# Performance work log

Hardware: AMD Instinct MI355X
Metric: run time of the kernel (lower is better)

Reference implementation:

```python
import jax, jax.numpy as jnp
import numpy as np
import math

N_NODES = 50000
N_EDGES = 800000
F_IN = 32
HID = 64


def _layernorm(x, g, b, eps=1e-5):
    mu = x.mean(-1, keepdims=True)
    var = ((x - mu) ** 2).mean(-1, keepdims=True)
    return (x - mu) / jnp.sqrt(var + eps) * g + b


def _tconv(x, src, dst, Wq, bq, Wk, bk, Wv, bv, Ws, heads):
    # PyG TransformerConv (concat=True, root_weight=True, bias=False on skip)
    N = x.shape[0]
    C = Wq.shape[1] // heads
    q = (x @ Wq + bq).reshape(N, heads, C)[dst]  # [E,H,C] gathered at targets
    k = (x @ Wk + bk).reshape(N, heads, C)[src]  # [E,H,C] gathered at sources
    v = (x @ Wv + bv).reshape(N, heads, C)[src]
    scores = (q * k).sum(-1) / math.sqrt(C)      # [E,H]
    m = jax.ops.segment_max(scores, dst, num_segments=N)   # [N,H]
    p = jnp.exp(scores - m[dst])
    denom = jax.ops.segment_sum(p, dst, num_segments=N)
    alpha = p / (denom[dst] + 1e-16)             # segment softmax over in-edges
    agg = jax.ops.segment_sum(v * alpha[..., None], dst, num_segments=N)
    return agg.reshape(N, heads * C) + x @ Ws    # + skip (no bias)


def setup_inputs() -> dict:
    key = jax.random.key(0)
    ks = iter(jax.random.split(key, 64))
    def rn(shape, s=0.1):
        return jax.random.normal(next(ks), shape, jnp.float32) * s
    inp = {
        "x": rn((N_NODES, F_IN), 1.0),
        "edge_index": jax.random.randint(next(ks), (2, N_EDGES), 0, N_NODES, dtype=jnp.int32),
        "ln0_g": jnp.ones((F_IN,), jnp.float32),
        "ln0_b": jnp.zeros((F_IN,), jnp.float32),
    }
    dims = [F_IN, HID, HID]
    for l in range(3):
        d = dims[l]
        inp[f"Wq{l}"] = rn((d, HID)); inp[f"bq{l}"] = rn((HID,), 0.05)
        inp[f"Wk{l}"] = rn((d, HID)); inp[f"bk{l}"] = rn((HID,), 0.05)
        inp[f"Wv{l}"] = rn((d, HID)); inp[f"bv{l}"] = rn((HID,), 0.05)
        inp[f"Ws{l}"] = rn((d, HID))
        inp[f"g{l}"] = jnp.ones((HID,), jnp.float32)
        inp[f"b{l}"] = jnp.zeros((HID,), jnp.float32)
    inp["Wr1"] = rn((HID, HID // 2)); inp["br1"] = jnp.zeros((HID // 2,), jnp.float32)
    inp["Wr2"] = rn((HID // 2, 1));   inp["br2"] = jnp.zeros((1,), jnp.float32)
    inp["Wt1"] = rn((HID, HID // 2)); inp["bt1"] = jnp.zeros((HID // 2,), jnp.float32)
    inp["Wt2"] = rn((HID // 2, 1));   inp["bt2"] = jnp.zeros((1,), jnp.float32)
    return inp


def reference(x, edge_index, ln0_g, ln0_b,
              Wq0, bq0, Wk0, bk0, Wv0, bv0, Ws0, g0, b0,
              Wq1, bq1, Wk1, bk1, Wv1, bv1, Ws1, g1, b1,
              Wq2, bq2, Wk2, bk2, Wv2, bv2, Ws2, g2, b2,
              Wr1, br1, Wr2, br2, Wt1, bt1, Wt2, bt2):
    src, dst = edge_index[0], edge_index[1]
    h = _layernorm(x, ln0_g, ln0_b)
    layers = [
        (Wq0, bq0, Wk0, bk0, Wv0, bv0, Ws0, g0, b0, 4),
        (Wq1, bq1, Wk1, bk1, Wv1, bv1, Ws1, g1, b1, 4),
        (Wq2, bq2, Wk2, bk2, Wv2, bv2, Ws2, g2, b2, 1),
    ]
    for i, (Wq, bq, Wk, bk, Wv, bv, Ws, g, b, heads) in enumerate(layers):
        x_res = h if h.shape[-1] == HID else None
        h = _tconv(h, src, dst, Wq, bq, Wk, bk, Wv, bv, Ws, heads)
        h = _layernorm(h, g, b)
        if x_res is not None and i > 0:
            h = h + 0.1 * x_res
        if i < len(layers) - 1:
            h = jax.nn.relu(h)  # dropout is identity in eval mode
    rtt = jax.nn.relu(h @ Wr1 + br1) @ Wr2 + br2      # [N,1]
    retrans = jax.nn.relu(h @ Wt1 + bt1) @ Wt2 + bt2  # [N,1]
    return jnp.concatenate([rtt, retrans], axis=1)    # [N,2]
```

## Files before the change

kernel.cpp:

```cpp
#include <hip/hip_runtime.h>
#include <hip/hip_bf16.h>
#include <math.h>

#define N_NODES 50000
#define N_EDGES 800000
#define HID 64
#define NBK 196
#define EPB 1024
#define SB  782
#define FLAT (NBK * SB)
#define SCAN_B ((FLAT + 255) / 256)

#define LN0_BLKS   6250
#define HIST_BLKS  SB
#define WP0_BLKS   32
#define WP12_BLKS  64
#define PREP_BLKS  (LN0_BLKS + HIST_BLKS + WP0_BLKS + 2 * WP12_BLKS)

typedef __attribute__((ext_vector_type(8))) short short8;
typedef __attribute__((ext_vector_type(4))) float float4v;

__device__ __forceinline__ unsigned short f32_to_bf16_rne(float f) {
    unsigned int u = __float_as_uint(f);
    unsigned int r = u + 0x7fffu + ((u >> 16) & 1u);
    return (unsigned short)(r >> 16);
}

__device__ __forceinline__ void ln0_body(int b, int t,
        const float* __restrict__ x, const float* __restrict__ g,
        const float* __restrict__ bb, float* __restrict__ h0) {
    int lane = t & 63;
    int n = b * 8 + (t >> 6) * 2 + (lane >> 5);
    int c = lane & 31;
    float v = x[n * 32 + c];
    float s = v;
    #pragma unroll
    for (int off = 1; off < 32; off <<= 1) s += __shfl_xor(s, off);
    float mu = s * (1.0f / 32.0f);
    float d = v - mu;
    float vs = d * d;
    #pragma unroll
    for (int off = 1; off < 32; off <<= 1) vs += __shfl_xor(vs, off);
    float var = vs * (1.0f / 32.0f);
    h0[n * 32 + c] = d * rsqrtf(var + 1e-5f) * g[c] + bb[c];
}

__device__ __forceinline__ void wprep_body(int idx, int KS,
        const float* __restrict__ Wq, const float* __restrict__ Wk,
        const float* __restrict__ Wv, const float* __restrict__ Ws,
        unsigned short* __restrict__ Wp) {
    int j = idx & 7;
    int lane = (idx >> 3) & 63;
    int ts = idx >> 9;
    int s = ts % KS;
    int tile = ts / KS;
    int which = tile >> 2;
    int slice = tile & 3;
    int k = s * 32 + ((lane >> 4) * 8) + j;
    int col = slice * 16 + (lane & 15);
    const float* W = (which == 0) ? Wq : (which == 1) ? Wk : (which == 2) ? Wv : Ws;
    Wp[idx] = f32_to_bf16_rne(W[k * 64 + col]);
}

__global__ __launch_bounds__(256) void prep_kernel(
        const float* __restrict__ x, const float* __restrict__ ln0g,
        const float* __restrict__ ln0b, float* __restrict__ h0,
        const int* __restrict__ dst, int* __restrict__ ghist,
        const float* __restrict__ Wq0, const float* __restrict__ Wk0,
        const float* __restrict__ Wv0, const float* __restrict__ Ws0,
        unsigned short* __restrict__ Wp0,
        const float* __restrict__ Wq1, const float* __restrict__ Wk1,
        const float* __restrict__ Wv1, const float* __restrict__ Ws1,
        unsigned short* __restrict__ Wp1,
        const float* __restrict__ Wq2, const float* __restrict__ Wk2,
        const float* __restrict__ Wv2, const float* __restrict__ Ws2,
        unsigned short* __restrict__ Wp2) {
    __shared__ int hist[NBK];
    int b = blockIdx.x;
    int t = threadIdx.x;
    if (b < LN0_BLKS) {
        ln0_body(b, t, x, ln0g, ln0b, h0);
    } else if (b < LN0_BLKS + HIST_BLKS) {
        int i = b - LN0_BLKS;
        for (int k = t; k < NBK; k += 256) hist[k] = 0;
        __syncthreads();
        int e0 = i * EPB;
        #pragma unroll
        for (int r = 0; r < 4; r++) {
            int e = e0 + r * 256 + t;
            if (e < N_EDGES) atomicAdd(&hist[dst[e] >> 8], 1);
        }
        __syncthreads();
        for (int k = t; k < NBK; k += 256) ghist[k * SB + i] = hist[k];
    } else if (b < LN0_BLKS + HIST_BLKS + WP0_BLKS) {
        int idx = (b - LN0_BLKS - HIST_BLKS) * 256 + t;
        wprep_body(idx, 1, Wq0, Wk0, Wv0, Ws0, Wp0);
    } else if (b < LN0_BLKS + HIST_BLKS + WP0_BLKS + WP12_BLKS) {
        int idx = (b - LN0_BLKS - HIST_BLKS - WP0_BLKS) * 256 + t;
        wprep_body(idx, 2, Wq1, Wk1, Wv1, Ws1, Wp1);
    } else {
        int idx = (b - LN0_BLKS - HIST_BLKS - WP0_BLKS - WP12_BLKS) * 256 + t;
        wprep_body(idx, 2, Wq2, Wk2, Wv2, Ws2, Wp2);
    }
}

__global__ void scan1_kernel(const int* __restrict__ ghist, int* __restrict__ csum) {
    int f = blockIdx.x * 256 + threadIdx.x;
    int v = (f < FLAT) ? ghist[f] : 0;
    #pragma unroll
    for (int off = 1; off < 64; off <<= 1) v += __shfl_xor(v, off);
    __shared__ int ws[4];
    if ((threadIdx.x & 63) == 0) ws[threadIdx.x >> 6] = v;
    __syncthreads();
    if (threadIdx.x == 0) csum[blockIdx.x] = ws[0] + ws[1] + ws[2] + ws[3];
}

__global__ void scan2_kernel(const int* __restrict__ csum, int* __restrict__ coff,
                             int* __restrict__ bbase, int* __restrict__ row_ptr) {
    int lane = threadIdx.x;
    int carry = 0;
    for (int base = 0; base < SCAN_B; base += 64) {
        int i = base + lane;
        int v = (i < SCAN_B) ? csum[i] : 0;
        int incl = v;
        #pragma unroll
        for (int off = 1; off < 64; off <<= 1) {
            int tt = __shfl_up(incl, off);
            if (lane >= off) incl += tt;
        }
        if (i < SCAN_B) coff[i] = carry + incl - v;
        carry += __shfl(incl, 63);
    }
    if (lane == 0) { bbase[NBK] = N_EDGES; row_ptr[N_NODES] = N_EDGES; }
}

__global__ void scan3_kernel(const int* __restrict__ ghist, const int* __restrict__ coff,
                             int* __restrict__ goff, int* __restrict__ bbase) {
    int f = blockIdx.x * 256 + threadIdx.x;
    int lane = threadIdx.x & 63;
    int w = threadIdx.x >> 6;
    int v = (f < FLAT) ? ghist[f] : 0;
    int incl = v;
    #pragma unroll
    for (int off = 1; off < 64; off <<= 1) {
        int tt = __shfl_up(incl, off);
        if (lane >= off) incl += tt;
    }
    __shared__ int ws[4];
    if (lane == 63) ws[w] = incl;
    __syncthreads();
    int woff = 0;
    #pragma unroll
    for (int k = 0; k < 4; k++) if (k < w) woff += ws[k];
    int excl = coff[blockIdx.x] + woff + incl - v;
    if (f < FLAT) {
        goff[f] = excl;
        if (f % SB == 0) bbase[f / SB] = excl;
    }
}

__global__ __launch_bounds__(256) void scatter_kernel(
        const int* __restrict__ src, const int* __restrict__ dst,
        const int* __restrict__ goff, int2* __restrict__ ebkt) {
    __shared__ int hist[NBK];
    int t = threadIdx.x, i = blockIdx.x;
    for (int k = t; k < NBK; k += 256) hist[k] = 0;
    __syncthreads();
    int e0 = i * EPB;
    #pragma unroll
    for (int r = 0; r < 4; r++) {
        int e = e0 + r * 256 + t;
        if (e < N_EDGES) {
            int s = src[e], d = dst[e];
            int k = d >> 8;
            int rank = atomicAdd(&hist[k], 1);
            ebkt[goff[k * SB + i] + rank] = make_int2(s, d);
        }
    }
}

__global__ __launch_bounds__(256) void bucket_build_kernel(
        const int2* __restrict__ ebkt, const int* __restrict__ bbase,
        int* __restrict__ row_ptr, int* __restrict__ colb) {
    __shared__ int ldeg[256];
    __shared__ int lcur[256];
    __shared__ int wsum[4];
    int b = blockIdx.x;
    int t = threadIdx.x;
    int cbase = bbase[b];
    int cnt = bbase[b + 1] - cbase;
    int ebase = cbase;

    ldeg[t] = 0;
    __syncthreads();
    for (int i = t; i < cnt; i += 256) {
        int2 e = ebkt[ebase + i];
        atomicAdd(&ldeg[e.y & 255], 1);
    }
    __syncthreads();

    int lane = t & 63;
    int w = t >> 6;
    int v = ldeg[t];
    int incl = v;
    #pragma unroll
    for (int off = 1; off < 64; off <<= 1) {
        int tt = __shfl_up(incl, off);
        if (lane >= off) incl += tt;
    }
    if (lane == 63) wsum[w] = incl;
    __syncthreads();
    int woff = 0;
    #pragma unroll
    for (int k = 0; k < 4; k++) if (k < w) woff += wsum[k];
    int excl = woff + incl - v;

    int node = b * 256 + t;
    if (node < N_NODES) row_ptr[node] = cbase + excl;
    lcur[t] = excl;
    __syncthreads();

    for (int i = t; i < cnt; i += 256) {
        int2 e = ebkt[ebase + i];
        int r = atomicAdd(&lcur[e.y & 255], 1);
        colb[cbase + r] = e.x;
    }
}

template <int D>
__global__ __launch_bounds__(256) void qkvs_mfma_kernel(
        const float* __restrict__ h,
        const unsigned short* __restrict__ Wp,
        const float* __restrict__ bq, const float* __restrict__ bk,
        const float* __restrict__ bv,
        float* __restrict__ Q, unsigned int* __restrict__ KV,
        float* __restrict__ S) {
    constexpr int KS = D / 32;
    int t = threadIdx.x;
    int lane = t & 63;
    int w = t >> 6;
    int n0 = blockIdx.x * 16;
    int n16 = lane & 15;
    int quad = lane >> 4;
    int col = w * 16 + n16;

    short8 afrag[KS];
    #pragma unroll
    for (int s = 0; s < KS; s++) {
        const float* hp = &h[(n0 + n16) * D + s * 32 + quad * 8];
        float4 a0 = *(const float4*)hp;
        float4 a1 = *(const float4*)(hp + 4);
        short8 af;
        af[0] = (short)f32_to_bf16_rne(a0.x);
        af[1] = (short)f32_to_bf16_rne(a0.y);
        af[2] = (short)f32_to_bf16_rne(a0.z);
        af[3] = (short)f32_to_bf16_rne(a0.w);
        af[4] = (short)f32_to_bf16_rne(a1.x);
        af[5] = (short)f32_to_bf16_rne(a1.y);
        af[6] = (short)f32_to_bf16_rne(a1.z);
        af[7] = (short)f32_to_bf16_rne(a1.w);
        afrag[s] = af;
    }

    float4v accs[4];
    #pragma unroll
    for (int which = 0; which < 4; which++) {
        float4v acc = {0.0f, 0.0f, 0.0f, 0.0f};
        int tile = which * 4 + w;
        #pragma unroll
        for (int s = 0; s < KS; s++) {
            short8 bfrag = *(const short8*)&Wp[((tile * KS + s) * 64 + lane) * 8];
            acc = __builtin_amdgcn_mfma_f32_16x16x32_bf16(afrag[s], bfrag, acc, 0, 0, 0);
        }
        accs[which] = acc;
    }

    float bqc = bq[col], bkc = bk[col], bvc = bv[col];

    #pragma unroll
    for (int r = 0; r < 4; r++) {
        int node = n0 + quad * 4 + r;
        Q[node * 64 + col] = accs[0][r] + bqc;
        unsigned int kw = f32_to_bf16_rne(accs[1][r] + bkc);
        unsigned int vw = f32_to_bf16_rne(accs[2][r] + bvc);
        KV[node * 64 + col] = (vw << 16) | kw;
        S[node * 64 + col] = accs[3][r];
    }
}

template <int HEADS, bool RES, bool RELU, bool HEAD>
__global__ __launch_bounds__(256) void agg_kernel(
                           const float* __restrict__ Q, const unsigned int* __restrict__ KV,
                           const float* __restrict__ S,
                           const int* __restrict__ row_ptr, const int* __restrict__ colb,
                           const float* __restrict__ g, const float* __restrict__ b,
                           const float* __restrict__ h_in, float* __restrict__ h_out,
                           const float* __restrict__ Wr1, const float* __restrict__ br1,
                           const float* __restrict__ Wr2, const float* __restrict__ br2,
                           const float* __restrict__ Wt1, const float* __restrict__ bt1,
                           const float* __restrict__ Wt2, const float* __restrict__ bt2,
                           float* __restrict__ out) {
    constexpr int C = HID / HEADS;
    int lane = threadIdx.x & 63;
    int m = lane & 15;
    int grp = lane >> 4;
    int n = blockIdx.x * 4 + (threadIdx.x >> 6);

    const float scale = rsqrtf((float)C);
    float4 q4 = *(const float4*)&Q[n * 64 + 4 * m];
    q4.x *= scale; q4.y *= scale; q4.z *= scale; q4.w *= scale;

    int beg = row_ptr[n], end = row_ptr[n + 1];

    float ssum = 0.0f;
    float acc0 = 0.0f, acc1 = 0.0f, acc2 = 0.0f, acc3 = 0.0f;

    for (int base = beg; base < end; base += 64) {
        int limit = min(end - base, 64);
        int src_l = (base + lane < end) ? colb[base + lane] : 0;
        for (int sub = 0; sub < limit; sub += 16) {
            int e0 = sub + grp, e1 = sub + 4 + grp, e2 = sub + 8 + grp, e3 = sub + 12 + grp;
            int s0 = __shfl(src_l, e0);
            int s1 = __shfl(src_l, e1);
            int s2 = __shfl(src_l, e2);
            int s3 = __shfl(src_l, e3);
            bool v0ok = e0 < limit, v1ok = e1 < limit, v2ok = e2 < limit, v3ok = e3 < limit;
            uint4 kv0 = make_uint4(0, 0, 0, 0), kv1 = kv0, kv2 = kv0, kv3 = kv0;
            if (v0ok) kv0 = *(const uint4*)&KV[(size_t)s0 * 64 + 4 * m];
            if (v1ok) kv1 = *(const uint4*)&KV[(size_t)s1 * 64 + 4 * m];
            if (v2ok) kv2 = *(const uint4*)&KV[(size_t)s2 * 64 + 4 * m];
            if (v3ok) kv3 = *(const uint4*)&KV[(size_t)s3 * 64 + 4 * m];

            float t0 = fmaf(q4.x, __uint_as_float(kv0.x << 16),
                       fmaf(q4.y, __uint_as_float(kv0.y << 16),
                       fmaf(q4.z, __uint_as_float(kv0.z << 16),
                            q4.w * __uint_as_float(kv0.w << 16))));
            float t1 = fmaf(q4.x, __uint_as_float(kv1.x << 16),
                       fmaf(q4.y, __uint_as_float(kv1.y << 16),
                       fmaf(q4.z, __uint_as_float(kv1.z << 16),
                            q4.w * __uint_as_float(kv1.w << 16))));
            float t2 = fmaf(q4.x, __uint_as_float(kv2.x << 16),
                       fmaf(q4.y, __uint_as_float(kv2.y << 16),
                       fmaf(q4.z, __uint_as_float(kv2.z << 16),
                            q4.w * __uint_as_float(kv2.w << 16))));
            float t3 = fmaf(q4.x, __uint_as_float(kv3.x << 16),
                       fmaf(q4.y, __uint_as_float(kv3.y << 16),
                       fmaf(q4.z, __uint_as_float(kv3.z << 16),
                            q4.w * __uint_as_float(kv3.w << 16))));
            #pragma unroll
            for (int off = 1; off < C / 4; off <<= 1) {
                t0 += __shfl_xor(t0, off);
                t1 += __shfl_xor(t1, off);
                t2 += __shfl_xor(t2, off);
                t3 += __shfl_xor(t3, off);
            }
            float p0 = v0ok ? __expf(t0) : 0.0f;
            float p1 = v1ok ? __expf(t1) : 0.0f;
            float p2 = v2ok ? __expf(t2) : 0.0f;
            float p3 = v3ok ? __expf(t3) : 0.0f;
            ssum += (p0 + p1) + (p2 + p3);
            acc0 = fmaf(p0, __uint_as_float(kv0.x & 0xffff0000u),
                   fmaf(p1, __uint_as_float(kv1.x & 0xffff0000u),
                   fmaf(p2, __uint_as_float(kv2.x & 0xffff0000u),
                   fmaf(p3, __uint_as_float(kv3.x & 0xffff0000u), acc0))));
            acc1 = fmaf(p0, __uint_as_float(kv0.y & 0xffff0000u),
                   fmaf(p1, __uint_as_float(kv1.y & 0xffff0000u),
                   fmaf(p2, __uint_as_float(kv2.y & 0xffff0000u),
                   fmaf(p3, __uint_as_float(kv3.y & 0xffff0000u), acc1))));
            acc2 = fmaf(p0, __uint_as_float(kv0.z & 0xffff0000u),
                   fmaf(p1, __uint_as_float(kv1.z & 0xffff0000u),
                   fmaf(p2, __uint_as_float(kv2.z & 0xffff0000u),
                   fmaf(p3, __uint_as_float(kv3.z & 0xffff0000u), acc2))));
            acc3 = fmaf(p0, __uint_as_float(kv0.w & 0xffff0000u),
                   fmaf(p1, __uint_as_float(kv1.w & 0xffff0000u),
                   fmaf(p2, __uint_as_float(kv2.w & 0xffff0000u),
                   fmaf(p3, __uint_as_float(kv3.w & 0xffff0000u), acc3))));
        }
    }

    #pragma unroll
    for (int off = 16; off < 64; off <<= 1) {
        ssum += __shfl_xor(ssum, off);
        acc0 += __shfl_xor(acc0, off);
        acc1 += __shfl_xor(acc1, off);
        acc2 += __shfl_xor(acc2, off);
        acc3 += __shfl_xor(acc3, off);
    }

    float inv = 1.0f / (ssum + 1e-16f);
    float4 sv = *(const float4*)&S[n * 64 + 4 * m];
    float o0 = fmaf(acc0, inv, sv.x);
    float o1 = fmaf(acc1, inv, sv.y);
    float o2 = fmaf(acc2, inv, sv.z);
    float o3 = fmaf(acc3, inv, sv.w);

    float s = (o0 + o1) + (o2 + o3);
    #pragma unroll
    for (int off = 1; off < 16; off <<= 1) s += __shfl_xor(s, off);
    float mu = s * (1.0f / 64.0f);
    float d0 = o0 - mu, d1 = o1 - mu, d2 = o2 - mu, d3 = o3 - mu;
    float vs = (d0 * d0 + d1 * d1) + (d2 * d2 + d3 * d3);
    #pragma unroll
    for (int off = 1; off < 16; off <<= 1) vs += __shfl_xor(vs, off);
    float rstd = rsqrtf(vs * (1.0f / 64.0f) + 1e-5f);

    float4 gv = *(const float4*)&g[4 * m];
    float4 bv = *(const float4*)&b[4 * m];
    float y0 = d0 * rstd * gv.x + bv.x;
    float y1 = d1 * rstd * gv.y + bv.y;
    float y2 = d2 * rstd * gv.z + bv.z;
    float y3 = d3 * rstd * gv.w + bv.w;
    if (RES) {
        float4 rv = *(const float4*)&h_in[n * 64 + 4 * m];
        y0 = fmaf(0.1f, rv.x, y0);
        y1 = fmaf(0.1f, rv.y, y1);
        y2 = fmaf(0.1f, rv.z, y2);
        y3 = fmaf(0.1f, rv.w, y3);
    }
    if (RELU) {
        y0 = fmaxf(y0, 0.0f); y1 = fmaxf(y1, 0.0f);
        y2 = fmaxf(y2, 0.0f); y3 = fmaxf(y3, 0.0f);
    }

    if (!HEAD) {
        if (grp == 0) {
            float4 yv = make_float4(y0, y1, y2, y3);
            *(float4*)&h_out[n * 64 + 4 * m] = yv;
        }
    } else {
        __shared__ float sh[4][HID];
        int wave = threadIdx.x >> 6;
        if (grp == 0) {
            float4 yv = make_float4(y0, y1, y2, y3);
            *(float4*)&sh[wave][4 * m] = yv;
        }
        __syncthreads();
        int half = lane >> 5;
        int j = lane & 31;
        const float* W1 = half ? Wt1 : Wr1;
        const float* b1 = half ? bt1 : br1;
        const float* W2 = half ? Wt2 : Wr2;
        const float* b2v = half ? bt2 : br2;
        float a = b1[j];
        #pragma unroll 8
        for (int i = 0; i < 64; i++) a = fmaf(sh[wave][i], W1[i * 32 + j], a);
        a = fmaxf(a, 0.0f);
        float r = a * W2[j];
        #pragma unroll
        for (int off = 1; off < 32; off <<= 1) r += __shfl_xor(r, off);
        if (j == 0) out[n * 2 + half] = r + b2v[0];
    }
}

extern "C" void kernel_launch(void* const* d_in, const int* in_sizes, int n_in,
                              void* d_out, int out_size, void* d_ws, size_t ws_size,
                              hipStream_t stream) {
    const float* x    = (const float*)d_in[0];
    const int*   ei   = (const int*)d_in[1];
    const int*   src  = ei;
    const int*   dst  = ei + N_EDGES;
    const float* ln0g = (const float*)d_in[2];
    const float* ln0b = (const float*)d_in[3];

    const float* P[27];
    for (int i = 0; i < 27; i++) P[i] = (const float*)d_in[4 + i];
    const float* Wr1 = (const float*)d_in[31];
    const float* br1 = (const float*)d_in[32];
    const float* Wr2 = (const float*)d_in[33];
    const float* br2 = (const float*)d_in[34];
    const float* Wt1 = (const float*)d_in[35];
    const float* bt1 = (const float*)d_in[36];
    const float* Wt2 = (const float*)d_in[37];
    const float* bt2 = (const float*)d_in[38];

    float* out = (float*)d_out;

    float* hbuf0 = (float*)d_ws;
    float* hbuf1 = hbuf0 + N_NODES * 64;
    float* Qb    = hbuf1 + N_NODES * 64;
    float* Sb    = Qb + N_NODES * 64;
    unsigned int* KVb = (unsigned int*)(Sb + N_NODES * 64);
    int* row_ptr = (int*)(KVb + N_NODES * 64);
    int* colb    = row_ptr + (N_NODES + 1);
    int* ghist   = colb + N_EDGES;
    int* goff    = ghist + FLAT;
    int* csum    = goff + FLAT;
    int* coff    = csum + SCAN_B;
    int* bbase   = coff + SCAN_B;
    unsigned short* Wp0 = (unsigned short*)(bbase + NBK + 1);
    unsigned short* Wp1 = Wp0 + 16 * 1 * 512;
    unsigned short* Wp2 = Wp1 + 16 * 2 * 512;
    int2* ebkt = (int2*)Qb;

    prep_kernel<<<PREP_BLKS, 256, 0, stream>>>(x, ln0g, ln0b, hbuf0,
        dst, ghist,
        P[0],  P[2],  P[4],  P[6],  Wp0,
        P[9],  P[11], P[13], P[15], Wp1,
        P[18], P[20], P[22], P[24], Wp2);
    scan1_kernel<<<SCAN_B, 256, 0, stream>>>(ghist, csum);
    scan2_kernel<<<1, 64, 0, stream>>>(csum, coff, bbase, row_ptr);
    scan3_kernel<<<SCAN_B, 256, 0, stream>>>(ghist, coff, goff, bbase);
    scatter_kernel<<<SB, 256, 0, stream>>>(src, dst, goff, ebkt);
    bucket_build_kernel<<<NBK, 256, 0, stream>>>(ebkt, bbase, row_ptr, colb);

    qkvs_mfma_kernel<32><<<3125, 256, 0, stream>>>(hbuf0, Wp0,
        P[1], P[3], P[5], Qb, KVb, Sb);
    agg_kernel<4, false, true, false><<<12500, 256, 0, stream>>>(Qb, KVb, Sb,
        row_ptr, colb, P[7], P[8], nullptr, hbuf1,
        Wr1, br1, Wr2, br2, Wt1, bt1, Wt2, bt2, out);

    qkvs_mfma_kernel<64><<<3125, 256, 0, stream>>>(hbuf1, Wp1,
        P[10], P[12], P[14], Qb, KVb, Sb);
    agg_kernel<4, true, true, false><<<12500, 256, 0, stream>>>(Qb, KVb, Sb,
        row_ptr, colb, P[16], P[17], hbuf1, hbuf0,
        Wr1, br1, Wr2, br2, Wt1, bt1, Wt2, bt2, out);

    qkvs_mfma_kernel<64><<<3125, 256, 0, stream>>>(hbuf0, Wp2,
        P[19], P[21], P[23], Qb, KVb, Sb);
    agg_kernel<1, true, false, true><<<12500, 256, 0, stream>>>(Qb, KVb, Sb,
        row_ptr, colb, P[25], P[26], hbuf0, hbuf1,
        Wr1, br1, Wr2, br2, Wt1, bt1, Wt2, bt2, out);
}
```

Baseline: 338.3 us.

## Fuse next-layer QKVS MFMA projection into aggregation kernel and merge scan kernels

The aggregation kernel for layers 0 and 1 now handles 16 nodes per 1024-thread block. It stages the normalized outputs in shared memory and then runs the next layer's bf16 MFMA Q/K/V/S projection in the same kernel, writing into a second ping-pong buffer set. This removes two qkvs launches and the round trip of re-reading h from global memory. The three-kernel histogram scan is replaced by a single-block scan, and the edges-per-block count rises to 4096, which shrinks the histogram. The costs are larger blocks with a syncthreads barrier that can lower occupancy during the gather phase, extra workspace, and a serial one-block scan.

New measurement: 355.6 us. 1.05x slower.

```diff
diff --git a/kernel.cpp b/kernel.cpp
--- a/kernel.cpp
+++ b/kernel.cpp
@@ -6,10 +6,9 @@
 #define N_EDGES 800000
 #define HID 64
 #define NBK 196
-#define EPB 1024
-#define SB  782
+#define EPB 4096
+#define SB  ((N_EDGES + EPB - 1) / EPB)
 #define FLAT (NBK * SB)
-#define SCAN_B ((FLAT + 255) / 256)
 
 #define LN0_BLKS   6250
 #define HIST_BLKS  SB
@@ -86,7 +85,7 @@
         __syncthreads();
         int e0 = i * EPB;
         #pragma unroll
-        for (int r = 0; r < 4; r++) {
+        for (int r = 0; r < EPB / 256; r++) {
             int e = e0 + r * 256 + t;
             if (e < N_EDGES) atomicAdd(&hist[dst[e] >> 8], 1);
         }
@@ -104,59 +103,41 @@
     }
 }
 
-__global__ void scan1_kernel(const int* __restrict__ ghist, int* __restrict__ csum) {
-    int f = blockIdx.x * 256 + threadIdx.x;
-    int v = (f < FLAT) ? ghist[f] : 0;
-    #pragma unroll
-    for (int off = 1; off < 64; off <<= 1) v += __shfl_xor(v, off);
-    __shared__ int ws[4];
-    if ((threadIdx.x & 63) == 0) ws[threadIdx.x >> 6] = v;
-    __syncthreads();
-    if (threadIdx.x == 0) csum[blockIdx.x] = ws[0] + ws[1] + ws[2] + ws[3];
-}
-
-__global__ void scan2_kernel(const int* __restrict__ csum, int* __restrict__ coff,
-                             int* __restrict__ bbase, int* __restrict__ row_ptr) {
-    int lane = threadIdx.x;
+__global__ __launch_bounds__(1024) void scan_all_kernel(
+        const int* __restrict__ ghist, int* __restrict__ goff,
+        int* __restrict__ bbase, int* __restrict__ row_ptr) {
+    __shared__ int wsum[16];
+    int t = threadIdx.x;
+    int lane = t & 63;
+    int w = t >> 6;
     int carry = 0;
-    for (int base = 0; base < SCAN_B; base += 64) {
-        int i = base + lane;
-        int v = (i < SCAN_B) ? csum[i] : 0;
+    for (int base = 0; base < FLAT; base += 1024) {
+        int f = base + t;
+        int v = (f < FLAT) ? ghist[f] : 0;
         int incl = v;
         #pragma unroll
         for (int off = 1; off < 64; off <<= 1) {
             int tt = __shfl_up(incl, off);
             if (lane >= off) incl += tt;
         }
-        if (i < SCAN_B) coff[i] = carry + incl - v;
-        carry += __shfl(incl, 63);
-    }
-    if (lane == 0) { bbase[NBK] = N_EDGES; row_ptr[N_NODES] = N_EDGES; }
-}
-
-__global__ void scan3_kernel(const int* __restrict__ ghist, const int* __restrict__ coff,
-                             int* __restrict__ goff, int* __restrict__ bbase) {
-    int f = blockIdx.x * 256 + threadIdx.x;
-    int lane = threadIdx.x & 63;
-    int w = threadIdx.x >> 6;
-    int v = (f < FLAT) ? ghist[f] : 0;
-    int incl = v;
-    #pragma unroll
-    for (int off = 1; off < 64; off <<= 1) {
-        int tt = __shfl_up(incl, off);
-        if (lane >= off) incl += tt;
-    }
-    __shared__ int ws[4];
-    if (lane == 63) ws[w] = incl;
-    __syncthreads();
-    int woff = 0;
-    #pragma unroll
-    for (int k = 0; k < 4; k++) if (k < w) woff += ws[k];
-    int excl = coff[blockIdx.x] + woff + incl - v;
-    if (f < FLAT) {
-        goff[f] = excl;
-        if (f % SB == 0) bbase[f / SB] = excl;
-    }
+        if (lane == 63) wsum[w] = incl;
+        __syncthreads();
+        int woff = 0, total = 0;
+        #pragma unroll
+        for (int k = 0; k < 16; k++) {
+            int s = wsum[k];
+            total += s;
+            if (k < w) woff += s;
+        }
+        int excl = carry + woff + incl - v;
+        if (f < FLAT) {
+            goff[f] = excl;
+            if (f % SB == 0) bbase[f / SB] = excl;
+        }
+        carry += total;
+        __syncthreads();
+    }
+    if (t == 0) { bbase[NBK] = N_EDGES; row_ptr[N_NODES] = N_EDGES; }
 }
 
 __global__ __launch_bounds__(256) void scatter_kernel(
@@ -168,7 +149,7 @@
     __syncthreads();
     int e0 = i * EPB;
     #pragma unroll
-    for (int r = 0; r < 4; r++) {
+    for (int r = 0; r < EPB / 256; r++) {
         int e = e0 + r * 256 + t;
         if (e < N_EDGES) {
             int s = src[e], d = dst[e];
@@ -189,12 +170,11 @@
     int t = threadIdx.x;
     int cbase = bbase[b];
     int cnt = bbase[b + 1] - cbase;
-    int ebase = cbase;
 
     ldeg[t] = 0;
     __syncthreads();
     for (int i = t; i < cnt; i += 256) {
-        int2 e = ebkt[ebase + i];
+        int2 e = ebkt[cbase + i];
         atomicAdd(&ldeg[e.y & 255], 1);
     }
     __syncthreads();
@@ -221,7 +201,7 @@
     __syncthreads();
 
     for (int i = t; i < cnt; i += 256) {
-        int2 e = ebkt[ebase + i];
+        int2 e = ebkt[cbase + i];
         int r = atomicAdd(&lcur[e.y & 255], 1);
         colb[cbase + r] = e.x;
     }
@@ -288,23 +268,26 @@
     }
 }
 
-template <int HEADS, bool RES, bool RELU, bool HEAD>
-__global__ __launch_bounds__(256) void agg_kernel(
-                           const float* __restrict__ Q, const unsigned int* __restrict__ KV,
-                           const float* __restrict__ S,
-                           const int* __restrict__ row_ptr, const int* __restrict__ colb,
-                           const float* __restrict__ g, const float* __restrict__ b,
-                           const float* __restrict__ h_in, float* __restrict__ h_out,
-                           const float* __restrict__ Wr1, const float* __restrict__ br1,
-                           const float* __restrict__ Wr2, const float* __restrict__ br2,
-                           const float* __restrict__ Wt1, const float* __restrict__ bt1,
-                           const float* __restrict__ Wt2, const float* __restrict__ bt2,
-                           float* __restrict__ out) {
+template <int HEADS, bool RES, bool RELU>
+__global__ __launch_bounds__(1024) void aggq_kernel(
+        const float* __restrict__ Q, const unsigned int* __restrict__ KV,
+        const float* __restrict__ S,
+        const int* __restrict__ row_ptr, const int* __restrict__ colb,
+        const float* __restrict__ g, const float* __restrict__ b,
+        const float* __restrict__ h_in, float* __restrict__ h_out,
+        const unsigned short* __restrict__ Wpn,
+        const float* __restrict__ bqn, const float* __restrict__ bkn,
+        const float* __restrict__ bvn,
+        float* __restrict__ Qn, unsigned int* __restrict__ KVn,
+        float* __restrict__ Sn) {
     constexpr int C = HID / HEADS;
+    __shared__ float sh[16][68];
     int lane = threadIdx.x & 63;
     int m = lane & 15;
     int grp = lane >> 4;
-    int n = blockIdx.x * 4 + (threadIdx.x >> 6);
+    int wave = threadIdx.x >> 6;
+    int n0 = blockIdx.x * 16;
+    int n = n0 + wave;
 
     const float scale = rsqrtf((float)C);
     float4 q4 = *(const float4*)&Q[n * 64 + 4 * m];
@@ -421,35 +404,214 @@
         y0 = fmaxf(y0, 0.0f); y1 = fmaxf(y1, 0.0f);
         y2 = fmaxf(y2, 0.0f); y3 = fmaxf(y3, 0.0f);
     }
-
-    if (!HEAD) {
-        if (grp == 0) {
-            float4 yv = make_float4(y0, y1, y2, y3);
-            *(float4*)&h_out[n * 64 + 4 * m] = yv;
-        }
-    } else {
-        __shared__ float sh[4][HID];
-        int wave = threadIdx.x >> 6;
-        if (grp == 0) {
-            float4 yv = make_float4(y0, y1, y2, y3);
-            *(float4*)&sh[wave][4 * m] = yv;
-        }
-        __syncthreads();
-        int half = lane >> 5;
-        int j = lane & 31;
-        const float* W1 = half ? Wt1 : Wr1;
-        const float* b1 = half ? bt1 : br1;
-        const float* W2 = half ? Wt2 : Wr2;
-        const float* b2v = half ? bt2 : br2;
-        float a = b1[j];
-        #pragma unroll 8
-        for (int i = 0; i < 64; i++) a = fmaf(sh[wave][i], W1[i * 32 + j], a);
-        a = fmaxf(a, 0.0f);
-        float r = a * W2[j];
+    if (grp == 0) {
+        float4 yv = make_float4(y0, y1, y2, y3);
+        *(float4*)&sh[wave][4 * m] = yv;
+        *(float4*)&h_out[n * 64 + 4 * m] = yv;
+    }
+    __syncthreads();
+
+    if (threadIdx.x < 256) {
+        int tt = threadIdx.x;
+        int lane2 = tt & 63;
+        int w4 = tt >> 6;
+        int n16 = lane2 & 15;
+        int quad2 = lane2 >> 4;
+        int col = w4 * 16 + n16;
+
+        short8 afrag[2];
         #pragma unroll
-        for (int off = 1; off < 32; off <<= 1) r += __shfl_xor(r, off);
-        if (j == 0) out[n * 2 + half] = r + b2v[0];
-    }
+        for (int sI = 0; sI < 2; sI++) {
+            float4 a0 = *(const float4*)&sh[n16][sI * 32 + quad2 * 8];
+            float4 a1 = *(const float4*)&sh[n16][sI * 32 + quad2 * 8 + 4];
+            short8 af;
+            af[0] = (short)f32_to_bf16_rne(a0.x);
+            af[1] = (short)f32_to_bf16_rne(a0.y);
+            af[2] = (short)f32_to_bf16_rne(a0.z);
+            af[3] = (short)f32_to_bf16_rne(a0.w);
+            af[4] = (short)f32_to_bf16_rne(a1.x);
+            af[5] = (short)f32_to_bf16_rne(a1.y);
+            af[6] = (short)f32_to_bf16_rne(a1.z);
+            af[7] = (short)f32_to_bf16_rne(a1.w);
+            afrag[sI] = af;
+        }
+
+        float4v accs[4];
+        #pragma unroll
+        for (int which = 0; which < 4; which++) {
+            float4v acc = {0.0f, 0.0f, 0.0f, 0.0f};
+            int tile = which * 4 + w4;
+            #pragma unroll
+            for (int sI = 0; sI < 2; sI++) {
+                short8 bfrag = *(const short8*)&Wpn[((tile * 2 + sI) * 64 + lane2) * 8];
+                acc = __builtin_amdgcn_mfma_f32_16x16x32_bf16(afrag[sI], bfrag, acc, 0, 0, 0);
+            }
+            accs[which] = acc;
+        }
+
+        float bqc = bqn[col], bkc = bkn[col], bvc = bvn[col];
+        #pragma unroll
+        for (int r = 0; r < 4; r++) {
+            int node = n0 + quad2 * 4 + r;
+            Qn[node * 64 + col] = accs[0][r] + bqc;
+            unsigned int kw = f32_to_bf16_rne(accs[1][r] + bkc);
+            unsigned int vw = f32_to_bf16_rne(accs[2][r] + bvc);
+            KVn[node * 64 + col] = (vw << 16) | kw;
+            Sn[node * 64 + col] = accs[3][r];
+        }
+    }
+}
+
+__global__ __launch_bounds__(256) void agg_head_kernel(
+        const float* __restrict__ Q, const unsigned int* __restrict__ KV,
+        const float* __restrict__ S,
+        const int* __restrict__ row_ptr, const int* __restrict__ colb,
+        const float* __restrict__ g, const float* __restrict__ b,
+        const float* __restrict__ h_in,
+        const float* __restrict__ Wr1, const float* __restrict__ br1,
+        const float* __restrict__ Wr2, const float* __restrict__ br2,
+        const float* __restrict__ Wt1, const float* __restrict__ bt1,
+        const float* __restrict__ Wt2, const float* __restrict__ bt2,
+        float* __restrict__ out) {
+    constexpr int C = 64;
+    __shared__ float sh[4][HID];
+    int lane = threadIdx.x & 63;
+    int m = lane & 15;
+    int grp = lane >> 4;
+    int wave = threadIdx.x >> 6;
+    int n = blockIdx.x * 4 + wave;
+
+    const float scale = rsqrtf((float)C);
+    float4 q4 = *(const float4*)&Q[n * 64 + 4 * m];
+    q4.x *= scale; q4.y *= scale; q4.z *= scale; q4.w *= scale;
+
+    int beg = row_ptr[n], end = row_ptr[n + 1];
+
+    float ssum = 0.0f;
+    float acc0 = 0.0f, acc1 = 0.0f, acc2 = 0.0f, acc3 = 0.0f;
+
+    for (int base = beg; base < end; base += 64) {
+        int limit = min(end - base, 64);
+        int src_l = (base + lane < end) ? colb[base + lane] : 0;
+        for (int sub = 0; sub < limit; sub += 16) {
+            int e0 = sub + grp, e1 = sub + 4 + grp, e2 = sub + 8 + grp, e3 = sub + 12 + grp;
+            int s0 = __shfl(src_l, e0);
+            int s1 = __shfl(src_l, e1);
+            int s2 = __shfl(src_l, e2);
+            int s3 = __shfl(src_l, e3);
+            bool v0ok = e0 < limit, v1ok = e1 < limit, v2ok = e2 < limit, v3ok = e3 < limit;
+            uint4 kv0 = make_uint4(0, 0, 0, 0), kv1 = kv0, kv2 = kv0, kv3 = kv0;
+            if (v0ok) kv0 = *(const uint4*)&KV[(size_t)s0 * 64 + 4 * m];
+            if (v1ok) kv1 = *(const uint4*)&KV[(size_t)s1 * 64 + 4 * m];
+            if (v2ok) kv2 = *(const uint4*)&KV[(size_t)s2 * 64 + 4 * m];
+            if (v3ok) kv3 = *(const uint4*)&KV[(size_t)s3 * 64 + 4 * m];
+
+            float t0 = fmaf(q4.x, __uint_as_float(kv0.x << 16),
+                       fmaf(q4.y, __uint_as_float(kv0.y << 16),
+                       fmaf(q4.z, __uint_as_float(kv0.z << 16),
+                            q4.w * __uint_as_float(kv0.w << 16))));
+            float t1 = fmaf(q4.x, __uint_as_float(kv1.x << 16),
+                       fmaf(q4.y, __uint_as_float(kv1.y << 16),
+                       fmaf(q4.z, __uint_as_float(kv1.z << 16),
+                            q4.w * __uint_as_float(kv1.w << 16))));
+            float t2 = fmaf(q4.x, __uint_as_float(kv2.x << 16),
+                       fmaf(q4.y, __uint_as_float(kv2.y << 16),
+                       fmaf(q4.z, __uint_as_float(kv2.z << 16),
+                            q4.w * __uint_as_float(kv2.w << 16))));
+            float t3 = fmaf(q4.x, __uint_as_float(kv3.x << 16),
+                       fmaf(q4.y, __uint_as_float(kv3.y << 16),
+                       fmaf(q4.z, __uint_as_float(kv3.z << 16),
+                            q4.w * __uint_as_float(kv3.w << 16))));
+            #pragma unroll
+            for (int off = 1; off < C / 4; off <<= 1) {
+                t0 += __shfl_xor(t0, off);
+                t1 += __shfl_xor(t1, off);
+                t2 += __shfl_xor(t2, off);
+                t3 += __shfl_xor(t3, off);
+            }
+            float p0 = v0ok ? __expf(t0) : 0.0f;
+            float p1 = v1ok ? __expf(t1) : 0.0f;
+            float p2 = v2ok ? __expf(t2) : 0.0f;
+            float p3 = v3ok ? __expf(t3) : 0.0f;
+            ssum += (p0 + p1) + (p2 + p3);
+            acc0 = fmaf(p0, __uint_as_float(kv0.x & 0xffff0000u),
+                   fmaf(p1, __uint_as_float(kv1.x & 0xffff0000u),
+                   fmaf(p2, __uint_as_float(kv2.x & 0xffff0000u),
+                   fmaf(p3, __uint_as_float(kv3.x & 0xffff0000u), acc0))));
+            acc1 = fmaf(p0, __uint_as_float(kv0.y & 0xffff0000u),
+                   fmaf(p1, __uint_as_float(kv1.y & 0xffff0000u),
+                   fmaf(p2, __uint_as_float(kv2.y & 0xffff0000u),
+                   fmaf(p3, __uint_as_float(kv3.y & 0xffff0000u), acc1))));
+            acc2 = fmaf(p0, __uint_as_float(kv0.z & 0xffff0000u),
+                   fmaf(p1, __uint_as_float(kv1.z & 0xffff0000u),
+                   fmaf(p2, __uint_as_float(kv2.z & 0xffff0000u),
+                   fmaf(p3, __uint_as_float(kv3.z & 0xffff0000u), acc2))));
+            acc3 = fmaf(p0, __uint_as_float(kv0.w & 0xffff0000u),
+                   fmaf(p1, __uint_as_float(kv1.w & 0xffff0000u),
+                   fmaf(p2, __uint_as_float(kv2.w & 0xffff0000u),
+                   fmaf(p3, __uint_as_float(kv3.w & 0xffff0000u), acc3))));
+        }
+    }
+
+    #pragma unroll
+    for (int off = 16; off < 64; off <<= 1) {
+        ssum += __shfl_xor(ssum, off);
+        acc0 += __shfl_xor(acc0, off);
+        acc1 += __shfl_xor(acc1, off);
+        acc2 += __shfl_xor(acc2, off);
+        acc3 += __shfl_xor(acc3, off);
+    }
+
+    float inv = 1.0f / (ssum + 1e-16f);
+    float4 sv = *(const float4*)&S[n * 64 + 4 * m];
+    float o0 = fmaf(acc0, inv, sv.x);
+    float o1 = fmaf(acc1, inv, sv.y);
+    float o2 = fmaf(acc2, inv, sv.z);
+    float o3 = fmaf(acc3, inv, sv.w);
+
+    float s = (o0 + o1) + (o2 + o3);
+    #pragma unroll
+    for (int off = 1; off < 16; off <<= 1) s += __shfl_xor(s, off);
+    float mu = s * (1.0f / 64.0f);
+    float d0 = o0 - mu, d1 = o1 - mu, d2 = o2 - mu, d3 = o3 - mu;
+    float vs = (d0 * d0 + d1 * d1) + (d2 * d2 + d3 * d3);
+    #pragma unroll
+    for (int off = 1; off < 16; off <<= 1) vs += __shfl_xor(vs, off);
+    float rstd = rsqrtf(vs * (1.0f / 64.0f) + 1e-5f);
+
+    float4 gv = *(const float4*)&g[4 * m];
+    float4 bv = *(const float4*)&b[4 * m];
+    float y0 = d0 * rstd * gv.x + bv.x;
+    float y1 = d1 * rstd * gv.y + bv.y;
+    float y2 = d2 * rstd * gv.z + bv.z;
+    float y3 = d3 * rstd * gv.w + bv.w;
+    {
+        float4 rv = *(const float4*)&h_in[n * 64 + 4 * m];
+        y0 = fmaf(0.1f, rv.x, y0);
+        y1 = fmaf(0.1f, rv.y, y1);
+        y2 = fmaf(0.1f, rv.z, y2);
+        y3 = fmaf(0.1f, rv.w, y3);
+    }
+
+    if (grp == 0) {
+        float4 yv = make_float4(y0, y1, y2, y3);
+        *(float4*)&sh[wave][4 * m] = yv;
+    }
+    __syncthreads();
+    int half = lane >> 5;
+    int j = lane & 31;
+    const float* W1 = half ? Wt1 : Wr1;
+    const float* b1 = half ? bt1 : br1;
+    const float* W2 = half ? Wt2 : Wr2;
+    const float* b2v = half ? bt2 : br2;
+    float a = b1[j];
+    #pragma unroll 8
+    for (int i = 0; i < 64; i++) a = fmaf(sh[wave][i], W1[i * 32 + j], a);
+    a = fmaxf(a, 0.0f);
+    float r = a * W2[j];
+    #pragma unroll
+    for (int off = 1; off < 32; off <<= 1) r += __shfl_xor(r, off);
+    if (j == 0) out[n * 2 + half] = r + b2v[0];
 }
 
 extern "C" void kernel_launch(void* const* d_in, const int* in_sizes, int n_in,
@@ -477,47 +639,43 @@
 
     float* hbuf0 = (float*)d_ws;
     float* hbuf1 = hbuf0 + N_NODES * 64;
-    float* Qb    = hbuf1 + N_NODES * 64;
-    float* Sb    = Qb + N_NODES * 64;
-    unsigned int* KVb = (unsigned int*)(Sb + N_NODES * 64);
-    int* row_ptr = (int*)(KVb + N_NODES * 64);
+    float* QbA   = hbuf1 + N_NODES * 64;
+    float* SbA   = QbA + N_NODES * 64;
+    unsigned int* KVbA = (unsigned int*)(SbA + N_NODES * 64);
+    float* QbB   = (float*)(KVbA + N_NODES * 64);
+    float* SbB   = QbB + N_NODES * 64;
+    unsigned int* KVbB = (unsigned int*)(SbB + N_NODES * 64);
+    int* row_ptr = (int*)(KVbB + N_NODES * 64);
     int* colb    = row_ptr + (N_NODES + 1);
     int* ghist   = colb + N_EDGES;
     int* goff    = ghist + FLAT;
-    int* csum    = goff + FLAT;
-    int* coff    = csum + SCAN_B;
-    int* bbase   = coff + SCAN_B;
+    int* bbase   = goff + FLAT;
     unsigned short* Wp0 = (unsigned short*)(bbase + NBK + 1);
     unsigned short* Wp1 = Wp0 + 16 * 1 * 512;
     unsigned short* Wp2 = Wp1 + 16 * 2 * 512;
-    int2* ebkt = (int2*)Qb;
+    int2* ebkt = (int2*)QbA;
 
     prep_kernel<<<PREP_BLKS, 256, 0, stream>>>(x, ln0g, ln0b, hbuf0,
         dst, ghist,
         P[0],  P[2],  P[4],  P[6],  Wp0,
         P[9],  P[11], P[13], P[15], Wp1,
         P[18], P[20], P[22], P[24], Wp2);
-    scan1_kernel<<<SCAN_B, 256, 0, stream>>>(ghist, csum);
-    scan2_kernel<<<1, 64, 0, stream>>>(csum, coff, bbase, row_ptr);
-    scan3_kernel<<<SCAN_B, 256, 0, stream>>>(ghist, coff, goff, bbase);
+    scan_all_kernel<<<1, 1024, 0, stream>>>(ghist, goff, bbase, row_ptr);
     scatter_kernel<<<SB, 256, 0, stream>>>(src, dst, goff, ebkt);
     bucket_build_kernel<<<NBK, 256, 0, stream>>>(ebkt, bbase, row_ptr, colb);
 
     qkvs_mfma_kernel<32><<<3125, 256, 0, stream>>>(hbuf0, Wp0,
-        P[1], P[3], P[5], Qb, KVb, Sb);
-    agg_kernel<4, false, true, false><<<12500, 256, 0, stream>>>(Qb, KVb, Sb,
+        P[1], P[3], P[5], QbA, KVbA, SbA);
+
+    aggq_kernel<4, false, true><<<3125, 1024, 0, stream>>>(QbA, KVbA, SbA,
         row_ptr, colb, P[7], P[8], nullptr, hbuf1,
+        Wp1, P[10], P[12], P[14], QbB, KVbB, SbB);
+
+    aggq_kernel<4, true, true><<<3125, 1024, 0, stream>>>(QbB, KVbB, SbB,
+        row_ptr, colb, P[16], P[17], hbuf1, hbuf0,
+        Wp2, P[19], P[21], P[23], QbA, KVbA, SbA);
+
+    agg_head_kernel<<<12500, 256, 0, stream>>>(QbA, KVbA, SbA,
+        row_ptr, colb, P[25], P[26], hbuf0,
         Wr1, br1, Wr2, br2, Wt1, bt1, Wt2, bt2, out);
-
-    qkvs_mfma_kernel<64><<<3125, 256, 0, stream>>>(hbuf1, Wp1,
-        P[10], P[12], P[14], Qb, KVb, Sb);
-    agg_kernel<4, true, true, false><<<12500, 256, 0, stream>>>(Qb, KVb, Sb,
-        row_ptr, colb, P[16], P[17], hbuf1, hbuf0,
-        Wr1, br1, Wr2, br2, Wt1, bt1, Wt2, bt2, out);
-
-    qkvs_mfma_kernel<64><<<3125, 256, 0, stream>>>(hbuf0, Wp2,
-        P[19], P[21], P[23], Qb, KVb, Sb);
-    agg_kernel<1, true, false, true><<<12500, 256, 0, stream>>>(Qb, KVb, Sb,
-        row_ptr, colb, P[25], P[26], hbuf0, hbuf1,
-        Wr1, br1, Wr2, br2, Wt1, bt1, Wt2, bt2, out);
-}
+}
```

## Enlarge edge chunks per block and merge three scan kernels into one

Applied to the files above, without the earlier changes.

Edges per histogram/scatter block grow from 1024 to 4096, which cuts the number of chunks and shrinks the flat histogram about fourfold. The three-kernel scan (block sums, carry scan, final scan) becomes a single 1024-thread block that loops over the smaller histogram with a running carry. This removes two kernel launches and their intermediate buffers. The cost is a serial single-block scan and fewer, heavier blocks in the histogram and scatter stages, which lowers parallelism there.

Measured after the change: 363.1 us. 7.3% more time.

```diff
diff --git a/kernel.cpp b/kernel.cpp
--- a/kernel.cpp
+++ b/kernel.cpp
@@ -6,10 +6,9 @@
 #define N_EDGES 800000
 #define HID 64
 #define NBK 196
-#define EPB 1024
-#define SB  782
+#define EPB 4096
+#define SB  ((N_EDGES + EPB - 1) / EPB)
 #define FLAT (NBK * SB)
-#define SCAN_B ((FLAT + 255) / 256)
 
 #define LN0_BLKS   6250
 #define HIST_BLKS  SB
@@ -86,7 +85,7 @@
         __syncthreads();
         int e0 = i * EPB;
         #pragma unroll
-        for (int r = 0; r < 4; r++) {
+        for (int r = 0; r < EPB / 256; r++) {
             int e = e0 + r * 256 + t;
             if (e < N_EDGES) atomicAdd(&hist[dst[e] >> 8], 1);
         }
@@ -104,59 +103,41 @@
     }
 }
 
-__global__ void scan1_kernel(const int* __restrict__ ghist, int* __restrict__ csum) {
-    int f = blockIdx.x * 256 + threadIdx.x;
-    int v = (f < FLAT) ? ghist[f] : 0;
-    #pragma unroll
-    for (int off = 1; off < 64; off <<= 1) v += __shfl_xor(v, off);
-    __shared__ int ws[4];
-    if ((threadIdx.x & 63) == 0) ws[threadIdx.x >> 6] = v;
-    __syncthreads();
-    if (threadIdx.x == 0) csum[blockIdx.x] = ws[0] + ws[1] + ws[2] + ws[3];
-}
-
-__global__ void scan2_kernel(const int* __restrict__ csum, int* __restrict__ coff,
-                             int* __restrict__ bbase, int* __restrict__ row_ptr) {
-    int lane = threadIdx.x;
+__global__ __launch_bounds__(1024) void scan_all_kernel(
+        const int* __restrict__ ghist, int* __restrict__ goff,
+        int* __restrict__ bbase, int* __restrict__ row_ptr) {
+    __shared__ int wsum[16];
+    int t = threadIdx.x;
+    int lane = t & 63;
+    int w = t >> 6;
     int carry = 0;
-    for (int base = 0; base < SCAN_B; base += 64) {
-        int i = base + lane;
-        int v = (i < SCAN_B) ? csum[i] : 0;
+    for (int base = 0; base < FLAT; base += 1024) {
+        int f = base + t;
+        int v = (f < FLAT) ? ghist[f] : 0;
         int incl = v;
         #pragma unroll
         for (int off = 1; off < 64; off <<= 1) {
             int tt = __shfl_up(incl, off);
             if (lane >= off) incl += tt;
         }
-        if (i < SCAN_B) coff[i] = carry + incl - v;
-        carry += __shfl(incl, 63);
-    }
-    if (lane == 0) { bbase[NBK] = N_EDGES; row_ptr[N_NODES] = N_EDGES; }
-}
-
-__global__ void scan3_kernel(const int* __restrict__ ghist, const int* __restrict__ coff,
-                             int* __restrict__ goff, int* __restrict__ bbase) {
-    int f = blockIdx.x * 256 + threadIdx.x;
-    int lane = threadIdx.x & 63;
-    int w = threadIdx.x >> 6;
-    int v = (f < FLAT) ? ghist[f] : 0;
-    int incl = v;
-    #pragma unroll
-    for (int off = 1; off < 64; off <<= 1) {
-        int tt = __shfl_up(incl, off);
-        if (lane >= off) incl += tt;
-    }
-    __shared__ int ws[4];
-    if (lane == 63) ws[w] = incl;
-    __syncthreads();
-    int woff = 0;
-    #pragma unroll
-    for (int k = 0; k < 4; k++) if (k < w) woff += ws[k];
-    int excl = coff[blockIdx.x] + woff + incl - v;
-    if (f < FLAT) {
-        goff[f] = excl;
-        if (f % SB == 0) bbase[f / SB] = excl;
-    }
+        if (lane == 63) wsum[w] = incl;
+        __syncthreads();
+        int woff = 0, total = 0;
+        #pragma unroll
+        for (int k = 0; k < 16; k++) {
+            int s = wsum[k];
+            total += s;
+            if (k < w) woff += s;
+        }
+        int excl = carry + woff + incl - v;
+        if (f < FLAT) {
+            goff[f] = excl;
+            if (f % SB == 0) bbase[f / SB] = excl;
+        }
+        carry += total;
+        __syncthreads();
+    }
+    if (t == 0) { bbase[NBK] = N_EDGES; row_ptr[N_NODES] = N_EDGES; }
 }
 
 __global__ __launch_bounds__(256) void scatter_kernel(
@@ -168,7 +149,7 @@
     __syncthreads();
     int e0 = i * EPB;
     #pragma unroll
-    for (int r = 0; r < 4; r++) {
+    for (int r = 0; r < EPB / 256; r++) {
         int e = e0 + r * 256 + t;
         if (e < N_EDGES) {
             int s = src[e], d = dst[e];
@@ -189,12 +170,11 @@
     int t = threadIdx.x;
     int cbase = bbase[b];
     int cnt = bbase[b + 1] - cbase;
-    int ebase = cbase;
 
     ldeg[t] = 0;
     __syncthreads();
     for (int i = t; i < cnt; i += 256) {
-        int2 e = ebkt[ebase + i];
+        int2 e = ebkt[cbase + i];
         atomicAdd(&ldeg[e.y & 255], 1);
     }
     __syncthreads();
@@ -221,7 +201,7 @@
     __syncthreads();
 
     for (int i = t; i < cnt; i += 256) {
-        int2 e = ebkt[ebase + i];
+        int2 e = ebkt[cbase + i];
         int r = atomicAdd(&lcur[e.y & 255], 1);
         colb[cbase + r] = e.x;
     }
@@ -484,9 +464,7 @@
     int* colb    = row_ptr + (N_NODES + 1);
     int* ghist   = colb + N_EDGES;
     int* goff    = ghist + FLAT;
-    int* csum    = goff + FLAT;
-    int* coff    = csum + SCAN_B;
-    int* bbase   = coff + SCAN_B;
+    int* bbase   = goff + FLAT;
     unsigned short* Wp0 = (unsigned short*)(bbase + NBK + 1);
     unsigned short* Wp1 = Wp0 + 16 * 1 * 512;
     unsigned short* Wp2 = Wp1 + 16 * 2 * 512;
@@ -497,9 +475,7 @@
         P[0],  P[2],  P[4],  P[6],  Wp0,
         P[9],  P[11], P[13], P[15], Wp1,
         P[18], P[20], P[22], P[24], Wp2);
-    scan1_kernel<<<SCAN_B, 256, 0, stream>>>(ghist, csum);
-    scan2_kernel<<<1, 64, 0, stream>>>(csum, coff, bbase, row_ptr);
-    scan3_kernel<<<SCAN_B, 256, 0, stream>>>(ghist, coff, goff, bbase);
+    scan_all_kernel<<<1, 1024, 0, stream>>>(ghist, goff, bbase, row_ptr);
     scatter_kernel<<<SB, 256, 0, stream>>>(src, dst, goff, ebkt);
     bucket_build_kernel<<<NBK, 256, 0, stream>>>(ebkt, bbase, row_ptr, colb);
 
```
